# Performance work log

Hardware: AMD Instinct MI355X
Metric: run time of the kernel (lower is better)

## Reference

```python
import jax, jax.numpy as jnp
import numpy as np

BATCH = 8
NDATA = 8192
NPOINT = 1024
NSAMPLE = 32
RADIUS = 0.2
CFEAT = 64


def setup_inputs() -> dict:
    key = jax.random.key(0)
    k1, k2, k3 = jax.random.split(key, 3)
    new_xyz = jax.random.normal(k1, (BATCH, NPOINT, 3), dtype=jnp.float32)
    xyz = jax.random.normal(k2, (BATCH, NDATA, 3), dtype=jnp.float32)
    points = jax.random.normal(k3, (BATCH, NDATA, CFEAT), dtype=jnp.float32)
    return {"new_xyz": new_xyz, "xyz": xyz, "points": points}


def reference(new_xyz, xyz, points):
    # Pairwise distances from every centroid to every dataset point.
    # delta: [B, P, N, 3]
    delta = xyz[:, None, :, :] - new_xyz[:, :, None, :]
    dist = jnp.linalg.norm(delta, axis=-1)  # [B, P, N]

    # Sort by distance (the original does a full argsort per centroid).
    sorted_idx = jnp.argsort(dist, axis=-1).astype(jnp.int32)  # [B, P, N]
    sorted_d = jnp.take_along_axis(dist, sorted_idx, axis=-1)  # [B, P, N]

    # Nearest point index replaces out-of-radius slots.
    nearest = sorted_idx[:, :, 0:1]  # [B, P, 1]
    radius_idx = jnp.where(sorted_d < RADIUS, sorted_idx, nearest)
    idx = radius_idx[:, :, :NSAMPLE]  # [B, P, S] int32 (ndataset >= nsample)

    # Batched gathers: grouped_xyz [B, P, S, 3], grouped_points [B, P, S, C].
    grouped_xyz = jnp.take_along_axis(
        xyz[:, None, :, :], idx[..., None], axis=2)
    grouped_points = jnp.take_along_axis(
        points[:, None, :, :], idx[..., None], axis=2)
    new_points = jnp.concatenate([grouped_xyz, grouped_points], axis=-1)
    return (new_points, idx, grouped_xyz)
```

## Files before the change

### kernel.cpp

```cpp
#include <hip/hip_runtime.h>
#include <math.h>

typedef unsigned int   u32;
typedef unsigned long long u64;

#define BATCH   8
#define NDATA   8192
#define NPOINT  1024
#define NSAMPLE 32
#define CFEAT   64
#define ROWF    67
#define MAXCAND 128
#define QPB     4
#define TILE    512
#define DWT     (TILE*3)
#define NT      (NDATA/TILE)

#define OUT_IDX (BATCH*NPOINT*NSAMPLE*ROWF)
#define OUT_GX  (OUT_IDX + BATCH*NPOINT*NSAMPLE)

__device__ __forceinline__ float rnbf(float f) {
    u32 b = __float_as_uint(f);
    b += 0x7FFFu + ((b >> 16) & 1u);
    return __uint_as_float(b & 0xFFFF0000u);
}
__device__ __forceinline__ int clampidx(int v) {
    return (v < 0) ? 0 : (v > NDATA-1 ? NDATA-1 : v);
}

__global__ __launch_bounds__(256, 8)
void grouping_kernel(const float* __restrict__ new_xyz,
                     const float* __restrict__ xyz,
                     const float* __restrict__ points,
                     float* __restrict__ out, float T)
{
    __shared__ u32   tileb[2][DWT];
    __shared__ float cand_s[QPB][MAXCAND];
    __shared__ int   cand_i[QPB][MAXCAND];
    __shared__ int   sel[QPB][NSAMPLE];

    const int tid  = threadIdx.x;
    const int wv   = tid >> 6;
    const int lane = tid & 63;
    const int q    = blockIdx.x * QPB + wv;
    const int b    = q >> 10;

    if (lane < NSAMPLE) sel[wv][lane] = 0;

    const float qx = new_xyz[q*3 + 0];
    const float qy = new_xyz[q*3 + 1];
    const float qz = new_xyz[q*3 + 2];
    const float* bx = xyz + (size_t)b * NDATA * 3;
    const u32*   src = (const u32*)bx;

    #pragma unroll
    for (int k = 0; k < DWT/256; ++k)
        tileb[0][k*256 + tid] = src[k*256 + tid];
    __syncthreads();

    int n = 0;
    for (int t = 0; t < NT; ++t) {
        const int cur = t & 1, nxt = cur ^ 1;
        if (t + 1 < NT) {
            #pragma unroll
            for (int k = 0; k < DWT/256; ++k)
                tileb[nxt][k*256 + tid] = src[(t+1)*DWT + k*256 + tid];
        }
        #pragma unroll 2
        for (int u = 0; u < TILE/64; ++u) {
            int il = (u << 6) + lane;
            const u32* tb = &tileb[cur][il*3];
            float x = __uint_as_float(tb[0]);
            float y = __uint_as_float(tb[1]);
            float z = __uint_as_float(tb[2]);
            float dx = __fsub_rn(x, qx), dy = __fsub_rn(y, qy), dz = __fsub_rn(z, qz);
            float d2 = __fadd_rn(__fadd_rn(__fmul_rn(dx,dx), __fmul_rn(dy,dy)),
                                 __fmul_rn(dz,dz));
            bool cc = d2 < T;
            u64 m = __ballot(cc);
            if (m) {
                if (cc) {
                    int below = __builtin_amdgcn_mbcnt_hi((u32)(m >> 32),
                                 __builtin_amdgcn_mbcnt_lo((u32)m, 0));
                    int pos = n + below;
                    if (pos < MAXCAND) {
                        cand_s[wv][pos] = __fsqrt_rn(d2);
                        cand_i[wv][pos] = t*TILE + il;
                    }
                }
                n += (int)__popcll(m);
            }
        }
        __syncthreads();
    }

    int mini = 0;
    if (n == 0) {
        float mind = 3.402823466e38f; int mi = 0;
        for (int k = 0; k < NDATA/64; ++k) {
            int i = (k << 6) + lane;
            float dx = __fsub_rn(bx[i*3+0], qx);
            float dy = __fsub_rn(bx[i*3+1], qy);
            float dz = __fsub_rn(bx[i*3+2], qz);
            float d2 = __fadd_rn(__fadd_rn(__fmul_rn(dx,dx), __fmul_rn(dy,dy)),
                                 __fmul_rn(dz,dz));
            if (d2 < mind) { mind = d2; mi = i; }
        }
        float ms = __fsqrt_rn(mind);
        for (int off = 32; off; off >>= 1) {
            float os = __shfl_xor(ms, off);
            int   oi = __shfl_xor(mi, off);
            if (os < ms || (os == ms && oi < mi)) { ms = os; mi = oi; }
        }
        mini = mi;
    }

    __syncthreads();

    const int nj = n > MAXCAND ? MAXCAND : n;
    for (int kk = lane; kk < nj; kk += 64) {
        float sk = cand_s[wv][kk];
        int r = 0;
        for (int mm = 0; mm < nj; ++mm) {
            float sm = cand_s[wv][mm];
            r += (int)((sm < sk) | ((sm == sk) & (mm < kk)));
        }
        if (r < NSAMPLE) sel[wv][r] = clampidx(cand_i[wv][kk]);
    }
    __syncthreads();
    {
        const int nsel = nj < NSAMPLE ? nj : NSAMPLE;
        if (lane >= nsel && lane < NSAMPLE) {
            int pad = (nj > 0) ? sel[wv][0] : clampidx(mini);
            sel[wv][lane] = pad;
        }
    }
    __syncthreads();

    if (lane < NSAMPLE)
        out[OUT_IDX + (size_t)q*NSAMPLE + lane] = rnbf((float)sel[wv][lane]);

    for (int e = lane; e < NSAMPLE*3; e += 64) {
        int sR = e / 3, c2 = e - sR*3;
        int is = sel[wv][sR];
        out[OUT_GX + (size_t)q*(NSAMPLE*3) + e] = rnbf(bx[is*3 + c2]);
    }

    const float* prow = points + (size_t)b * NDATA * CFEAT;
    float* onp = out + (size_t)q * (NSAMPLE*ROWF);
    for (int e = lane; e < NSAMPLE*ROWF; e += 64) {
        int s  = e / ROWF;
        int c  = e - s*ROWF;
        int is = sel[wv][s];
        const float* ap = (c < 3) ? (bx + (size_t)is*3 + c)
                                  : (prow + (size_t)is*CFEAT + (c-3));
        onp[e] = rnbf(*ap);
    }
}

extern "C" void kernel_launch(void* const* d_in, const int* in_sizes, int n_in,
                              void* d_out, int out_size, void* d_ws, size_t ws_size,
                              hipStream_t stream) {
    union { u32 u; float f; } lo, hi, mid;
    lo.u = 0u; hi.f = 0.05f;
    while (hi.u - lo.u > 1u) {
        mid.u = lo.u + (hi.u - lo.u) / 2u;
        if (sqrtf(mid.f) >= 0.2f) hi.u = mid.u; else lo.u = mid.u;
    }
    float T = hi.f;

    grouping_kernel<<<(BATCH*NPOINT)/QPB, 256, 0, stream>>>(
        (const float*)d_in[0],
        (const float*)d_in[1],
        (const float*)d_in[2],
        (float*)d_out, T);
}
```

Before: 132.5 us.

## Process two queries per wavefront with SoA shared tiles and float4 reads

```diff
diff --git a/kernel.cpp b/kernel.cpp
--- a/kernel.cpp
+++ b/kernel.cpp
@@ -11,10 +11,12 @@
 #define CFEAT   64
 #define ROWF    67
 #define MAXCAND 128
-#define QPB     4
+#define QPW     2
+#define QPB     8
 #define TILE    512
 #define DWT     (TILE*3)
 #define NT      (NDATA/TILE)
+#define PLANE   516
 
 #define OUT_IDX (BATCH*NPOINT*NSAMPLE*ROWF)
 #define OUT_GX  (OUT_IDX + BATCH*NPOINT*NSAMPLE)
@@ -28,13 +30,13 @@
     return (v < 0) ? 0 : (v > NDATA-1 ? NDATA-1 : v);
 }
 
-__global__ __launch_bounds__(256, 8)
+__global__ __launch_bounds__(256, 4)
 void grouping_kernel(const float* __restrict__ new_xyz,
                      const float* __restrict__ xyz,
                      const float* __restrict__ points,
                      float* __restrict__ out, float T)
 {
-    __shared__ u32   tileb[2][DWT];
+    __shared__ __align__(16) float S[2][3*PLANE];
     __shared__ float cand_s[QPB][MAXCAND];
     __shared__ int   cand_i[QPB][MAXCAND];
     __shared__ int   sel[QPB][NSAMPLE];
@@ -42,119 +44,167 @@
     const int tid  = threadIdx.x;
     const int wv   = tid >> 6;
     const int lane = tid & 63;
-    const int q    = blockIdx.x * QPB + wv;
-    const int b    = q >> 10;
-
-    if (lane < NSAMPLE) sel[wv][lane] = 0;
-
-    const float qx = new_xyz[q*3 + 0];
-    const float qy = new_xyz[q*3 + 1];
-    const float qz = new_xyz[q*3 + 2];
+    const int q0   = blockIdx.x * QPB + wv * QPW;
+    const int b    = q0 >> 10;
+
+    sel[wv*QPW + (lane >> 5)][lane & 31] = 0;
+
+    float qx[QPW], qy[QPW], qz[QPW];
+    #pragma unroll
+    for (int j = 0; j < QPW; ++j) {
+        qx[j] = new_xyz[(q0+j)*3 + 0];
+        qy[j] = new_xyz[(q0+j)*3 + 1];
+        qz[j] = new_xyz[(q0+j)*3 + 2];
+    }
     const float* bx = xyz + (size_t)b * NDATA * 3;
-    const u32*   src = (const u32*)bx;
-
-    #pragma unroll
-    for (int k = 0; k < DWT/256; ++k)
-        tileb[0][k*256 + tid] = src[k*256 + tid];
-    __syncthreads();
-
-    int n = 0;
+
+    #pragma unroll
+    for (int k = 0; k < DWT/256; ++k) {
+        int w = k*256 + tid;
+        int p = w / 3, c = w - 3*p;
+        S[0][c*PLANE + p] = bx[w];
+    }
+    __syncthreads();
+
+    int n[QPW]; n[0] = 0; n[1] = 0;
     for (int t = 0; t < NT; ++t) {
         const int cur = t & 1, nxt = cur ^ 1;
         if (t + 1 < NT) {
             #pragma unroll
-            for (int k = 0; k < DWT/256; ++k)
-                tileb[nxt][k*256 + tid] = src[(t+1)*DWT + k*256 + tid];
-        }
-        #pragma unroll 2
-        for (int u = 0; u < TILE/64; ++u) {
-            int il = (u << 6) + lane;
-            const u32* tb = &tileb[cur][il*3];
-            float x = __uint_as_float(tb[0]);
-            float y = __uint_as_float(tb[1]);
-            float z = __uint_as_float(tb[2]);
-            float dx = __fsub_rn(x, qx), dy = __fsub_rn(y, qy), dz = __fsub_rn(z, qz);
-            float d2 = __fadd_rn(__fadd_rn(__fmul_rn(dx,dx), __fmul_rn(dy,dy)),
-                                 __fmul_rn(dz,dz));
-            bool cc = d2 < T;
-            u64 m = __ballot(cc);
-            if (m) {
-                if (cc) {
-                    int below = __builtin_amdgcn_mbcnt_hi((u32)(m >> 32),
-                                 __builtin_amdgcn_mbcnt_lo((u32)m, 0));
-                    int pos = n + below;
-                    if (pos < MAXCAND) {
-                        cand_s[wv][pos] = __fsqrt_rn(d2);
-                        cand_i[wv][pos] = t*TILE + il;
+            for (int k = 0; k < DWT/256; ++k) {
+                int w = k*256 + tid;
+                int p = w / 3, c = w - 3*p;
+                S[nxt][c*PLANE + p] = bx[(t+1)*DWT + w];
+            }
+        }
+        #pragma unroll
+        for (int u = 0; u < TILE/256; ++u) {
+            const float4 xv = ((const float4*)(S[cur]          ))[u*64 + lane];
+            const float4 yv = ((const float4*)(S[cur] +   PLANE))[u*64 + lane];
+            const float4 zv = ((const float4*)(S[cur] + 2*PLANE))[u*64 + lane];
+            float d2v[QPW][4];
+            u64   mv [QPW][4];
+            u64 ored = 0;
+            #pragma unroll
+            for (int j = 0; j < 4; ++j) {
+                float x = (&xv.x)[j], y = (&yv.x)[j], z = (&zv.x)[j];
+                #pragma unroll
+                for (int s = 0; s < QPW; ++s) {
+                    float dx = __fsub_rn(x, qx[s]);
+                    float dy = __fsub_rn(y, qy[s]);
+                    float dz = __fsub_rn(z, qz[s]);
+                    float d2 = __fadd_rn(__fadd_rn(__fmul_rn(dx,dx), __fmul_rn(dy,dy)),
+                                         __fmul_rn(dz,dz));
+                    d2v[s][j] = d2;
+                    u64 m = __ballot(d2 < T);
+                    mv[s][j] = m;
+                    ored |= m;
+                }
+            }
+            if (ored) {
+                #pragma unroll
+                for (int s = 0; s < QPW; ++s) {
+                    #pragma unroll
+                    for (int j = 0; j < 4; ++j) {
+                        u64 m = mv[s][j];
+                        if (m) {
+                            if (d2v[s][j] < T) {
+                                int below = __builtin_amdgcn_mbcnt_hi((u32)(m >> 32),
+                                             __builtin_amdgcn_mbcnt_lo((u32)m, 0));
+                                int pos = n[s] + below;
+                                if (pos < MAXCAND) {
+                                    cand_s[wv*QPW + s][pos] = __fsqrt_rn(d2v[s][j]);
+                                    cand_i[wv*QPW + s][pos] = t*TILE + u*256 + 4*lane + j;
+                                }
+                            }
+                            n[s] += (int)__popcll(m);
+                        }
                     }
                 }
-                n += (int)__popcll(m);
             }
         }
         __syncthreads();
     }
 
-    int mini = 0;
-    if (n == 0) {
-        float mind = 3.402823466e38f; int mi = 0;
-        for (int k = 0; k < NDATA/64; ++k) {
-            int i = (k << 6) + lane;
-            float dx = __fsub_rn(bx[i*3+0], qx);
-            float dy = __fsub_rn(bx[i*3+1], qy);
-            float dz = __fsub_rn(bx[i*3+2], qz);
-            float d2 = __fadd_rn(__fadd_rn(__fmul_rn(dx,dx), __fmul_rn(dy,dy)),
-                                 __fmul_rn(dz,dz));
-            if (d2 < mind) { mind = d2; mi = i; }
-        }
-        float ms = __fsqrt_rn(mind);
-        for (int off = 32; off; off >>= 1) {
-            float os = __shfl_xor(ms, off);
-            int   oi = __shfl_xor(mi, off);
-            if (os < ms || (os == ms && oi < mi)) { ms = os; mi = oi; }
-        }
-        mini = mi;
-    }
-
-    __syncthreads();
-
-    const int nj = n > MAXCAND ? MAXCAND : n;
-    for (int kk = lane; kk < nj; kk += 64) {
-        float sk = cand_s[wv][kk];
-        int r = 0;
-        for (int mm = 0; mm < nj; ++mm) {
-            float sm = cand_s[wv][mm];
-            r += (int)((sm < sk) | ((sm == sk) & (mm < kk)));
-        }
-        if (r < NSAMPLE) sel[wv][r] = clampidx(cand_i[wv][kk]);
-    }
-    __syncthreads();
-    {
+    int mini[QPW]; mini[0] = 0; mini[1] = 0;
+    #pragma unroll
+    for (int s = 0; s < QPW; ++s) {
+        if (n[s] == 0) {
+            float mind = 3.402823466e38f; int mi = 0;
+            for (int k = 0; k < NDATA/64; ++k) {
+                int i = (k << 6) + lane;
+                float dx = __fsub_rn(bx[i*3+0], qx[s]);
+                float dy = __fsub_rn(bx[i*3+1], qy[s]);
+                float dz = __fsub_rn(bx[i*3+2], qz[s]);
+                float d2 = __fadd_rn(__fadd_rn(__fmul_rn(dx,dx), __fmul_rn(dy,dy)),
+                                     __fmul_rn(dz,dz));
+                if (d2 < mind) { mind = d2; mi = i; }
+            }
+            float ms = __fsqrt_rn(mind);
+            for (int off = 32; off; off >>= 1) {
+                float os = __shfl_xor(ms, off);
+                int   oi = __shfl_xor(mi, off);
+                if (os < ms || (os == ms && oi < mi)) { ms = os; mi = oi; }
+            }
+            mini[s] = mi;
+        }
+    }
+
+    __syncthreads();
+
+    #pragma unroll
+    for (int s = 0; s < QPW; ++s) {
+        const int wq = wv*QPW + s;
+        const int nj = n[s] > MAXCAND ? MAXCAND : n[s];
+        for (int kk = lane; kk < nj; kk += 64) {
+            float sk = cand_s[wq][kk];
+            int   ik = cand_i[wq][kk];
+            int r = 0;
+            for (int mm = 0; mm < nj; ++mm) {
+                float sm = cand_s[wq][mm];
+                int   im = cand_i[wq][mm];
+                r += (int)((sm < sk) | ((sm == sk) & (im < ik)));
+            }
+            if (r < NSAMPLE) sel[wq][r] = clampidx(ik);
+        }
+    }
+    __syncthreads();
+    #pragma unroll
+    for (int s = 0; s < QPW; ++s) {
+        const int wq = wv*QPW + s;
+        const int nj = n[s] > MAXCAND ? MAXCAND : n[s];
         const int nsel = nj < NSAMPLE ? nj : NSAMPLE;
         if (lane >= nsel && lane < NSAMPLE) {
-            int pad = (nj > 0) ? sel[wv][0] : clampidx(mini);
-            sel[wv][lane] = pad;
-        }
-    }
-    __syncthreads();
-
-    if (lane < NSAMPLE)
-        out[OUT_IDX + (size_t)q*NSAMPLE + lane] = rnbf((float)sel[wv][lane]);
-
-    for (int e = lane; e < NSAMPLE*3; e += 64) {
-        int sR = e / 3, c2 = e - sR*3;
-        int is = sel[wv][sR];
-        out[OUT_GX + (size_t)q*(NSAMPLE*3) + e] = rnbf(bx[is*3 + c2]);
-    }
+            int pad = (nj > 0) ? sel[wq][0] : clampidx(mini[s]);
+            sel[wq][lane] = pad;
+        }
+    }
+    __syncthreads();
 
     const float* prow = points + (size_t)b * NDATA * CFEAT;
-    float* onp = out + (size_t)q * (NSAMPLE*ROWF);
-    for (int e = lane; e < NSAMPLE*ROWF; e += 64) {
-        int s  = e / ROWF;
-        int c  = e - s*ROWF;
-        int is = sel[wv][s];
-        const float* ap = (c < 3) ? (bx + (size_t)is*3 + c)
-                                  : (prow + (size_t)is*CFEAT + (c-3));
-        onp[e] = rnbf(*ap);
+    #pragma unroll
+    for (int s = 0; s < QPW; ++s) {
+        const int q  = q0 + s;
+        const int wq = wv*QPW + s;
+
+        if (lane < NSAMPLE)
+            out[OUT_IDX + (size_t)q*NSAMPLE + lane] = rnbf((float)sel[wq][lane]);
+
+        for (int e = lane; e < NSAMPLE*3; e += 64) {
+            int sR = e / 3, c2 = e - sR*3;
+            int is = sel[wq][sR];
+            out[OUT_GX + (size_t)q*(NSAMPLE*3) + e] = rnbf(bx[is*3 + c2]);
+        }
+
+        float* onp = out + (size_t)q * (NSAMPLE*ROWF);
+        for (int e = lane; e < NSAMPLE*ROWF; e += 64) {
+            int sR = e / ROWF;
+            int c2 = e - sR*ROWF;
+            int is = sel[wq][sR];
+            const float* ap = (c2 < 3) ? (bx + (size_t)is*3 + c2)
+                                       : (prow + (size_t)is*CFEAT + (c2-3));
+            onp[e] = rnbf(*ap);
+        }
     }
 }
 
```

After: 136.6 us. 3.0% more time.

## Transpose xyz tile to SoA planes in LDS and read float4 vectors

Applied to the files above, without the earlier changes.

```diff
diff --git a/kernel.cpp b/kernel.cpp
--- a/kernel.cpp
+++ b/kernel.cpp
@@ -15,6 +15,7 @@
 #define TILE    512
 #define DWT     (TILE*3)
 #define NT      (NDATA/TILE)
+#define PLANE   516
 
 #define OUT_IDX (BATCH*NPOINT*NSAMPLE*ROWF)
 #define OUT_GX  (OUT_IDX + BATCH*NPOINT*NSAMPLE)
@@ -34,7 +35,7 @@
                      const float* __restrict__ points,
                      float* __restrict__ out, float T)
 {
-    __shared__ u32   tileb[2][DWT];
+    __shared__ __align__(16) float S[2][3*PLANE];
     __shared__ float cand_s[QPB][MAXCAND];
     __shared__ int   cand_i[QPB][MAXCAND];
     __shared__ int   sel[QPB][NSAMPLE];
@@ -51,11 +52,13 @@
     const float qy = new_xyz[q*3 + 1];
     const float qz = new_xyz[q*3 + 2];
     const float* bx = xyz + (size_t)b * NDATA * 3;
-    const u32*   src = (const u32*)bx;
 
     #pragma unroll
-    for (int k = 0; k < DWT/256; ++k)
-        tileb[0][k*256 + tid] = src[k*256 + tid];
+    for (int k = 0; k < DWT/256; ++k) {
+        int w = k*256 + tid;
+        int p = w / 3, c = w - 3*p;
+        S[0][c*PLANE + p] = bx[w];
+    }
     __syncthreads();
 
     int n = 0;
@@ -63,32 +66,38 @@
         const int cur = t & 1, nxt = cur ^ 1;
         if (t + 1 < NT) {
             #pragma unroll
-            for (int k = 0; k < DWT/256; ++k)
-                tileb[nxt][k*256 + tid] = src[(t+1)*DWT + k*256 + tid];
+            for (int k = 0; k < DWT/256; ++k) {
+                int w = k*256 + tid;
+                int p = w / 3, c = w - 3*p;
+                S[nxt][c*PLANE + p] = bx[(t+1)*DWT + w];
+            }
         }
-        #pragma unroll 2
-        for (int u = 0; u < TILE/64; ++u) {
-            int il = (u << 6) + lane;
-            const u32* tb = &tileb[cur][il*3];
-            float x = __uint_as_float(tb[0]);
-            float y = __uint_as_float(tb[1]);
-            float z = __uint_as_float(tb[2]);
-            float dx = __fsub_rn(x, qx), dy = __fsub_rn(y, qy), dz = __fsub_rn(z, qz);
-            float d2 = __fadd_rn(__fadd_rn(__fmul_rn(dx,dx), __fmul_rn(dy,dy)),
-                                 __fmul_rn(dz,dz));
-            bool cc = d2 < T;
-            u64 m = __ballot(cc);
-            if (m) {
-                if (cc) {
-                    int below = __builtin_amdgcn_mbcnt_hi((u32)(m >> 32),
-                                 __builtin_amdgcn_mbcnt_lo((u32)m, 0));
-                    int pos = n + below;
-                    if (pos < MAXCAND) {
-                        cand_s[wv][pos] = __fsqrt_rn(d2);
-                        cand_i[wv][pos] = t*TILE + il;
+        #pragma unroll
+        for (int u = 0; u < TILE/256; ++u) {
+            const float4 xv = ((const float4*)(S[cur]          ))[u*64 + lane];
+            const float4 yv = ((const float4*)(S[cur] +   PLANE))[u*64 + lane];
+            const float4 zv = ((const float4*)(S[cur] + 2*PLANE))[u*64 + lane];
+            #pragma unroll
+            for (int j = 0; j < 4; ++j) {
+                float dx = __fsub_rn((&xv.x)[j], qx);
+                float dy = __fsub_rn((&yv.x)[j], qy);
+                float dz = __fsub_rn((&zv.x)[j], qz);
+                float d2 = __fadd_rn(__fadd_rn(__fmul_rn(dx,dx), __fmul_rn(dy,dy)),
+                                     __fmul_rn(dz,dz));
+                bool cc = d2 < T;
+                u64 m = __ballot(cc);
+                if (m) {
+                    if (cc) {
+                        int below = __builtin_amdgcn_mbcnt_hi((u32)(m >> 32),
+                                     __builtin_amdgcn_mbcnt_lo((u32)m, 0));
+                        int pos = n + below;
+                        if (pos < MAXCAND) {
+                            cand_s[wv][pos] = __fsqrt_rn(d2);
+                            cand_i[wv][pos] = t*TILE + u*256 + 4*lane + j;
+                        }
                     }
+                    n += (int)__popcll(m);
                 }
-                n += (int)__popcll(m);
             }
         }
         __syncthreads();
@@ -120,12 +129,14 @@
     const int nj = n > MAXCAND ? MAXCAND : n;
     for (int kk = lane; kk < nj; kk += 64) {
         float sk = cand_s[wv][kk];
+        int   ik = cand_i[wv][kk];
         int r = 0;
         for (int mm = 0; mm < nj; ++mm) {
             float sm = cand_s[wv][mm];
-            r += (int)((sm < sk) | ((sm == sk) & (mm < kk)));
+            int   im = cand_i[wv][mm];
+            r += (int)((sm < sk) | ((sm == sk) & (im < ik)));
         }
-        if (r < NSAMPLE) sel[wv][r] = clampidx(cand_i[wv][kk]);
+        if (r < NSAMPLE) sel[wv][r] = clampidx(ik);
     }
     __syncthreads();
     {
@@ -149,11 +160,11 @@
     const float* prow = points + (size_t)b * NDATA * CFEAT;
     float* onp = out + (size_t)q * (NSAMPLE*ROWF);
     for (int e = lane; e < NSAMPLE*ROWF; e += 64) {
-        int s  = e / ROWF;
-        int c  = e - s*ROWF;
-        int is = sel[wv][s];
-        const float* ap = (c < 3) ? (bx + (size_t)is*3 + c)
-                                  : (prow + (size_t)is*CFEAT + (c-3));
+        int sR = e / ROWF;
+        int c2 = e - sR*ROWF;
+        int is = sel[wv][sR];
+        const float* ap = (c2 < 3) ? (bx + (size_t)is*3 + c2)
+                                   : (prow + (size_t)is*CFEAT + (c2-3));
         onp[e] = rnbf(*ap);
     }
 }
```

Result: no change. 131.6 us (-0.7%).
